# Kernel optimization log

Hardware: AMD Instinct MI355X
Metric: run time of the kernel (lower is better)

The kernel has to match this reference:

```python
import jax, jax.numpy as jnp
import numpy as np

N_NODES = 50000
N_EDGES = 800000
IN_DIM, HID_DIM, N_CLASS = 128, 128, 2
DROPOUT_P = 0.5
NEG_SLOPE = 0.01  # F.leaky_relu default


def gcn_conv(x, src, dst, W, b, n_nodes):
    """PyG GCNConv: add self-loops, sym-normalize, aggregate, then bias."""
    loops = jnp.arange(n_nodes, dtype=src.dtype)
    s = jnp.concatenate([src, loops])
    d = jnp.concatenate([dst, loops])
    # degree on A + I (edge weights = 1), counted at destination
    deg = jax.ops.segment_sum(jnp.ones_like(d, dtype=x.dtype), d, num_segments=n_nodes)
    dis = jnp.where(deg > 0, jax.lax.rsqrt(deg), 0.0)  # deg^{-1/2}
    norm = dis[s] * dis[d]                               # [E+N]
    h = x @ W                                            # [N, out]
    msg = h[s] * norm[:, None]                           # gather + scale
    out = jax.ops.segment_sum(msg, d, num_segments=n_nodes)  # scatter-add
    return out + b


def dropout(x, p, key):
    keep = 1.0 - p
    mask = jax.random.bernoulli(key, keep, x.shape)
    return jnp.where(mask, x / keep, 0.0)


def setup_inputs() -> dict:
    key = jax.random.key(0)
    ks = jax.random.split(key, 8)
    x = jax.random.normal(ks[0], (N_NODES, IN_DIM), dtype=jnp.float32)
    edge_index = jax.random.randint(ks[1], (2, N_EDGES), 0, N_NODES, dtype=jnp.int64)
    def glorot(k, fin, fout):
        lim = np.sqrt(6.0 / (fin + fout)).astype(np.float32)
        return jax.random.uniform(k, (fin, fout), jnp.float32, -lim, lim)
    W1 = glorot(ks[2], IN_DIM, HID_DIM)
    W2 = glorot(ks[3], HID_DIM, HID_DIM)
    W3 = glorot(ks[4], HID_DIM, N_CLASS)
    b1 = jnp.zeros((HID_DIM,), jnp.float32)
    b2 = jnp.zeros((HID_DIM,), jnp.float32)
    b3 = jnp.zeros((N_CLASS,), jnp.float32)
    return {"x": x, "edge_index": edge_index, "W1": W1, "b1": b1,
            "W2": W2, "b2": b2, "W3": W3, "b3": b3}


def reference(x, edge_index, W1, b1, W2, b2, W3, b3):
    src, dst = edge_index[0], edge_index[1]
    n = x.shape[0]
    dkey = jax.random.key(42)
    k1, k2 = jax.random.split(dkey)
    h = gcn_conv(x, src, dst, W1, b1, n)
    h = jax.nn.leaky_relu(h, NEG_SLOPE)
    h = dropout(h, DROPOUT_P, k1)
    h = gcn_conv(h, src, dst, W2, b2, n)
    h = jax.nn.leaky_relu(h, NEG_SLOPE)
    h = dropout(h, DROPOUT_P, k2)
    h = gcn_conv(h, src, dst, W3, b3, n)
    return jax.nn.log_softmax(h, axis=1)
```

## Files before the change

kernel.cpp:

```cpp
#include <hip/hip_runtime.h>
#include <stdint.h>

#define N_NODES 50000
#define N_EDGES 800000
#define DIM     128
#define NB   196
#define CAP  8192
#define CHUNK 2048
#define NBLK 391
#define GCAP 4096
#define G3NODES 128
#define G3CAP 4096
#define ZBLK 98

typedef __attribute__((ext_vector_type(8))) unsigned short ushort8_t;
typedef __attribute__((ext_vector_type(8))) short bfrag;
typedef __attribute__((ext_vector_type(4))) float f32x4;

__host__ __device__ inline void threefry2x32(uint32_t k0, uint32_t k1,
                                             uint32_t x0, uint32_t x1,
                                             uint32_t& o0, uint32_t& o1) {
    uint32_t ks0 = k0, ks1 = k1, ks2 = k0 ^ k1 ^ 0x1BD11BDAu;
    uint32_t v0 = x0 + ks0, v1 = x1 + ks1;
#define TF_R(r) { v0 += v1; v1 = (v1 << (r)) | (v1 >> (32 - (r))); v1 ^= v0; }
    TF_R(13) TF_R(15) TF_R(26) TF_R(6)
    v0 += ks1; v1 += ks2 + 1u;
    TF_R(17) TF_R(29) TF_R(16) TF_R(24)
    v0 += ks2; v1 += ks0 + 2u;
    TF_R(13) TF_R(15) TF_R(26) TF_R(6)
    v0 += ks0; v1 += ks1 + 3u;
    TF_R(17) TF_R(29) TF_R(16) TF_R(24)
    v0 += ks1; v1 += ks2 + 4u;
    TF_R(13) TF_R(15) TF_R(26) TF_R(6)
    v0 += ks2; v1 += ks0 + 5u;
#undef TF_R
    o0 = v0; o1 = v1;
}

__device__ inline float drop_scale(uint32_t kk0, uint32_t kk1, uint32_t i) {
    uint32_t b0, b1;
    threefry2x32(kk0, kk1, 0u, i, b0, b1);
    uint32_t bits = b0 ^ b1;
    return (bits >> 31) ? 0.0f : 2.0f;
}

__device__ inline float bf2f(ushort u) {
    return __uint_as_float(((uint32_t)u) << 16);
}

__device__ inline ushort f2bf_rne(float f) {
    uint32_t bits = __float_as_uint(f);
    uint32_t lsb = (bits >> 16) & 1u;
    bits += 0x7fffu + lsb;
    return (ushort)(bits >> 16);
}

template<int F32A, int SCALE>
__device__ inline void gemm_body(const ushort* __restrict__ Xb,
                                 const float* __restrict__ Xf,
                                 const ushort* __restrict__ Wt,
                                 const float* __restrict__ dis,
                                 ushort* __restrict__ Hb, int gb, int tid) {
    int w = tid >> 6, lane = tid & 63;
    int m0 = gb * 128 + w * 32;
    int lrow = lane & 15, quad = lane >> 4;
    f32x4 acc[2][8] = {};
    for (int kt = 0; kt < DIM; kt += 32) {
        bfrag a[2], b[8];
        #pragma unroll
        for (int t = 0; t < 2; ++t) {
            int m = m0 + t * 16 + lrow;
            if (m >= N_NODES) m = 0;
            if (F32A) {
                const float* p = Xf + (size_t)m * DIM + kt + quad * 8;
                f32x4 v0 = *(const f32x4*)p;
                f32x4 v1 = *(const f32x4*)(p + 4);
                #pragma unroll
                for (int j = 0; j < 4; ++j) {
                    a[t][j]     = (short)f2bf_rne(v0[j]);
                    a[t][j + 4] = (short)f2bf_rne(v1[j]);
                }
            } else {
                a[t] = *(const bfrag*)(Xb + (size_t)m * DIM + kt + quad * 8);
            }
        }
        #pragma unroll
        for (int c = 0; c < 8; ++c) {
            int n = c * 16 + lrow;
            b[c] = *(const bfrag*)(Wt + (size_t)n * DIM + kt + quad * 8);
        }
        #pragma unroll
        for (int t = 0; t < 2; ++t)
            #pragma unroll
            for (int c = 0; c < 8; ++c)
                acc[t][c] = __builtin_amdgcn_mfma_f32_16x16x32_bf16(a[t], b[c], acc[t][c], 0, 0, 0);
    }
    #pragma unroll
    for (int t = 0; t < 2; ++t) {
        #pragma unroll
        for (int r = 0; r < 4; ++r) {
            int rowi = m0 + t * 16 + quad * 4 + r;
            if (rowi < N_NODES) {
                float dv = SCALE ? dis[rowi] : 1.0f;
                #pragma unroll
                for (int c = 0; c < 8; ++c) {
                    int feat = c * 16 + lrow;
                    int fp = feat >> 5, off = feat & 31;
                    float z = SCALE ? acc[t][c][r] * dv : acc[t][c][r];
                    Hb[((size_t)fp * N_NODES + rowi) * 32 + off] = f2bf_rne(z);
                }
            }
        }
    }
}

__global__ __launch_bounds__(256) void k_prep(const float* __restrict__ W1,
                                              const float* __restrict__ W2,
                                              ushort* __restrict__ W1t,
                                              ushort* __restrict__ W2t,
                                              const int* __restrict__ src,
                                              const int* __restrict__ dst,
                                              uint32_t* __restrict__ gcur,
                                              uint32_t* __restrict__ packed,
                                              float* __restrict__ h3s) {
    __shared__ uint32_t h[NB];
    int b = blockIdx.x;
    int t = threadIdx.x;
    if (b < NBLK) {
        uint32_t dc[CHUNK / 256], sc[CHUNK / 256];
        if (t < NB) h[t] = 0u;
        __syncthreads();
        int base = b * CHUNK;
        #pragma unroll
        for (int i = 0; i < CHUNK / 256; ++i) {
            int e = base + i * 256 + t;
            if (e < N_EDGES) {
                dc[i] = (uint32_t)dst[e];
                sc[i] = (uint32_t)src[e];
                atomicAdd(&h[dc[i] >> 8], 1u);
            } else {
                dc[i] = 0xffffffffu;
            }
        }
        __syncthreads();
        if (t < NB) {
            uint32_t c = h[t];
            h[t] = c ? atomicAdd(&gcur[t], c) : 0u;
        }
        __syncthreads();
        #pragma unroll
        for (int i = 0; i < CHUNK / 256; ++i) {
            if (dc[i] != 0xffffffffu) {
                uint32_t d = dc[i];
                uint32_t s = sc[i];
                uint32_t bk = d >> 8;
                uint32_t pos = atomicAdd(&h[bk], 1u);
                if (pos < CAP)
                    packed[(size_t)bk * CAP + pos] = ((d & 255u) << 16) | s;
            }
        }
    } else if (b < NBLK + 128) {
        int j = (b - NBLK) * 256 + t;
        const float* W = (j < DIM * DIM) ? W1 : W2;
        ushort* Wt = (j < DIM * DIM) ? W1t : W2t;
        int i = j & (DIM * DIM - 1);
        int k = i >> 7, n = i & 127;
        Wt[n * DIM + k] = f2bf_rne(W[k * DIM + n]);
    } else {
        int idx = (b - NBLK - 128) * 256 + t;
        if (idx < (N_NODES * 2) / 4) {
            f32x4 z = {0.f, 0.f, 0.f, 0.f};
            ((f32x4*)h3s)[idx] = z;
        }
    }
}

__global__ __launch_bounds__(256) void k_fill(const uint32_t* __restrict__ gcur,
                                              const uint32_t* __restrict__ packed,
                                              uint32_t* __restrict__ row,
                                              float* __restrict__ dis,
                                              ushort* __restrict__ col16,
                                              const float* __restrict__ x,
                                              const ushort* __restrict__ W1t,
                                              ushort* __restrict__ Hb) {
    __shared__ uint32_t sdeg[256];
    __shared__ uint32_t scan[256];
    __shared__ uint32_t cur[256];
    int b = blockIdx.x;
    int t = threadIdx.x;
    if (b >= NB) {
        gemm_body<1, 0>(nullptr, x, W1t, nullptr, Hb, b - NB, t);
        return;
    }
    uint32_t n = gcur[b];
    scan[t] = (t < b) ? gcur[t] : 0u;
    __syncthreads();
    for (int off = 1; off < 256; off <<= 1) {
        uint32_t xx = (t >= off) ? scan[t - off] : 0u;
        __syncthreads();
        scan[t] += xx;
        __syncthreads();
    }
    uint32_t cbase = scan[255];
    __syncthreads();
    uint32_t pbase = (uint32_t)b * CAP;
    sdeg[t] = 0u;
    __syncthreads();
    for (uint32_t i = t; i < n; i += 256) {
        uint32_t u = packed[pbase + i];
        atomicAdd(&sdeg[u >> 16], 1u);
    }
    __syncthreads();
    uint32_t myd = sdeg[t];
    scan[t] = myd;
    __syncthreads();
    for (int off = 1; off < 256; off <<= 1) {
        uint32_t xx = (t >= off) ? scan[t - off] : 0u;
        __syncthreads();
        scan[t] += xx;
        __syncthreads();
    }
    uint32_t excl = scan[t] - myd;
    cur[t] = excl;
    int v = b * 256 + t;
    if (v <= N_NODES) row[v] = cbase + excl;
    if (v < N_NODES)  dis[v] = 1.0f / sqrtf((float)(myd + 1u));
    __syncthreads();
    for (uint32_t i = t; i < n; i += 256) {
        uint32_t u = packed[pbase + i];
        uint32_t pos = cbase + atomicAdd(&cur[u >> 16], 1u);
        col16[pos] = (ushort)(u & 0xffffu);
    }
}

template<int CLS, int SRCDIS>
__global__ __launch_bounds__(256) void k_gather_t(const uint32_t* __restrict__ row,
                                                  const ushort* __restrict__ col16,
                                                  const float* __restrict__ dis,
                                                  const ushort* __restrict__ Hb,
                                                  const float* __restrict__ bias,
                                                  ushort* __restrict__ OUTb,
                                                  const float* __restrict__ W3,
                                                  float* __restrict__ h3s,
                                                  uint32_t kk0, uint32_t kk1) {
    __shared__ ushort scol[GCAP];
    __shared__ uint32_t srow[65];
    int fp = blockIdx.x & 3;
    int c = blockIdx.x >> 2;
    int tid = threadIdx.x;
    int nbase = c * 64;
    int nend = nbase + 64; if (nend > N_NODES) nend = N_NODES;
    int nloc = nend - nbase;
    for (int i = tid; i <= nloc; i += 256) srow[i] = row[nbase + i];
    __syncthreads();
    uint32_t eLo = srow[0];
    uint32_t count = srow[nloc] - eLo;
    bool staged = count <= GCAP;
    if (staged) {
        for (uint32_t i = tid; i < count; i += 256) scol[i] = col16[eLo + i];
    }
    __syncthreads();

    int nl = tid >> 2;
    int q  = tid & 3;
    int v = nbase + nl;
    if (v >= N_NODES) return;
    float dv = dis[v];
    const ushort* Hf = Hb + (size_t)fp * N_NODES * 32;
    ushort8_t hv = *((const ushort8_t*)(Hf + (size_t)v * 32 + q * 8));
    float acc[8];
    #pragma unroll
    for (int j = 0; j < 8; ++j)
        acc[j] = SRCDIS ? dv * bf2f(hv[j]) : bf2f(hv[j]);

    uint32_t e0 = srow[nl] - eLo, e1 = srow[nl + 1] - eLo;
    uint32_t e = e0;
    if (staged) {
        for (; e + 4 <= e1; e += 4) {
            uint32_t s0 = scol[e], s1 = scol[e + 1], s2 = scol[e + 2], s3 = scol[e + 3];
            ushort8_t h0 = *((const ushort8_t*)(Hf + (size_t)s0 * 32 + q * 8));
            ushort8_t h1 = *((const ushort8_t*)(Hf + (size_t)s1 * 32 + q * 8));
            ushort8_t h2 = *((const ushort8_t*)(Hf + (size_t)s2 * 32 + q * 8));
            ushort8_t h3 = *((const ushort8_t*)(Hf + (size_t)s3 * 32 + q * 8));
            if (SRCDIS) {
                float d0 = dis[s0], d1 = dis[s1], d2 = dis[s2], d3 = dis[s3];
                #pragma unroll
                for (int j = 0; j < 8; ++j)
                    acc[j] += d0 * bf2f(h0[j]) + d1 * bf2f(h1[j])
                            + d2 * bf2f(h2[j]) + d3 * bf2f(h3[j]);
            } else {
                #pragma unroll
                for (int j = 0; j < 8; ++j)
                    acc[j] += (bf2f(h0[j]) + bf2f(h1[j])) + (bf2f(h2[j]) + bf2f(h3[j]));
            }
        }
        for (; e < e1; ++e) {
            uint32_t s0 = scol[e];
            ushort8_t h0 = *((const ushort8_t*)(Hf + (size_t)s0 * 32 + q * 8));
            float d0 = SRCDIS ? dis[s0] : 1.0f;
            #pragma unroll
            for (int j = 0; j < 8; ++j)
                acc[j] += SRCDIS ? d0 * bf2f(h0[j]) : bf2f(h0[j]);
        }
    } else {
        for (; e < e1; ++e) {
            uint32_t s0 = col16[eLo + e];
            ushort8_t h0 = *((const ushort8_t*)(Hf + (size_t)s0 * 32 + q * 8));
            float d0 = SRCDIS ? dis[s0] : 1.0f;
            #pragma unroll
            for (int j = 0; j < 8; ++j)
                acc[j] += SRCDIS ? d0 * bf2f(h0[j]) : bf2f(h0[j]);
        }
    }

    int cbase = fp * 32 + q * 8;
    uint32_t ibase = (uint32_t)(v * DIM + cbase);
    if (CLS == 0) {
        ushort8_t o;
        #pragma unroll
        for (int j = 0; j < 8; ++j) {
            float z = acc[j] * dv + bias[cbase + j];
            z = (z >= 0.f) ? z : 0.01f * z;
            z *= drop_scale(kk0, kk1, ibase + j);
            o[j] = f2bf_rne(z);
        }
        *((ushort8_t*)(OUTb + (size_t)v * DIM + cbase)) = o;
    } else {
        float o0 = 0.f, o1 = 0.f;
        #pragma unroll
        for (int j = 0; j < 8; ++j) {
            float z = acc[j] * dv + bias[cbase + j];
            z = (z >= 0.f) ? z : 0.01f * z;
            z *= drop_scale(kk0, kk1, ibase + j);
            o0 += z * W3[(cbase + j) * 2 + 0];
            o1 += z * W3[(cbase + j) * 2 + 1];
        }
        o0 += __shfl_xor(o0, 1); o0 += __shfl_xor(o0, 2);
        o1 += __shfl_xor(o1, 1); o1 += __shfl_xor(o1, 2);
        if (q == 0) {
            atomicAdd(&h3s[v * 2 + 0], o0 * dv);
            atomicAdd(&h3s[v * 2 + 1], o1 * dv);
        }
    }
}

__global__ __launch_bounds__(256) void k_gemm_bf16(const ushort* __restrict__ Xb,
                                                   const ushort* __restrict__ Wt,
                                                   const float* __restrict__ dis,
                                                   ushort* __restrict__ Hb) {
    gemm_body<0, 1>(Xb, nullptr, Wt, dis, Hb, blockIdx.x, threadIdx.x);
}

__global__ __launch_bounds__(256) void k_gather3(const uint32_t* __restrict__ row,
                                                 const ushort* __restrict__ col16,
                                                 const float* __restrict__ dis,
                                                 const float* __restrict__ H3s,
                                                 const float* __restrict__ b3,
                                                 float* __restrict__ out) {
    __shared__ ushort scol[G3CAP];
    __shared__ uint32_t srow[G3NODES + 1];
    int tid = threadIdx.x;
    int nbase = blockIdx.x * G3NODES;
    int nend = nbase + G3NODES; if (nend > N_NODES) nend = N_NODES;
    int nloc = nend - nbase;
    for (int i = tid; i <= nloc; i += 256) srow[i] = row[nbase + i];
    __syncthreads();
    uint32_t eLo = srow[0];
    uint32_t count = srow[nloc] - eLo;
    bool staged = count <= G3CAP;
    if (staged) {
        for (uint32_t i = tid; i < count; i += 256) scol[i] = col16[eLo + i];
    }
    __syncthreads();

    int nl = tid >> 1;
    int par = tid & 1;
    int v = nbase + nl;
    if (v >= N_NODES) return;
    const float2* H2 = (const float2*)H3s;
    float z0 = 0.f, z1 = 0.f;
    if (par == 0) {
        float2 h = H2[v];
        z0 = h.x; z1 = h.y;
    }
    uint32_t e0 = srow[nl] - eLo, e1 = srow[nl + 1] - eLo;
    if (staged) {
        for (uint32_t e = e0 + par; e < e1; e += 2) {
            float2 ha = H2[scol[e]];
            z0 += ha.x; z1 += ha.y;
        }
    } else {
        for (uint32_t e = e0 + par; e < e1; e += 2) {
            float2 ha = H2[col16[eLo + e]];
            z0 += ha.x; z1 += ha.y;
        }
    }
    z0 += __shfl_xor(z0, 1);
    z1 += __shfl_xor(z1, 1);
    if (par) return;
    float dv = dis[v];
    z0 = z0 * dv + b3[0];
    z1 = z1 * dv + b3[1];
    float m = fmaxf(z0, z1);
    float lse = m + logf(expf(z0 - m) + expf(z1 - m));
    out[v * 2 + 0] = z0 - lse;
    out[v * 2 + 1] = z1 - lse;
}

extern "C" void kernel_launch(void* const* d_in, const int* in_sizes, int n_in,
                              void* d_out, int out_size, void* d_ws, size_t ws_size,
                              hipStream_t stream) {
    const float* x  = (const float*)d_in[0];
    const int*   ei = (const int*)d_in[1];
    const float* W1 = (const float*)d_in[2];
    const float* b1 = (const float*)d_in[3];
    const float* W2 = (const float*)d_in[4];
    const float* b2 = (const float*)d_in[5];
    const float* W3 = (const float*)d_in[6];
    const float* b3 = (const float*)d_in[7];
    float* out = (float*)d_out;

    const int* src = ei;
    const int* dst = ei + N_EDGES;

    uint32_t* wsu = (uint32_t*)d_ws;
    float*    wsf = (float*)d_ws;
    uint32_t* gcur   = wsu;
    uint32_t* row    = wsu + 256;
    float*    dis    = wsf + 50304;
    uint32_t* packed = wsu + 100352;
    ushort*   col16  = (ushort*)(wsu + 1705984);
    ushort*   Hb     = (ushort*)(wsu + 2106112);
    ushort*   Bb     = (ushort*)(wsu + 8506112);
    ushort*   W1t    = (ushort*)(wsu + 11706112);
    ushort*   W2t    = (ushort*)(wsu + 11714304);
    float*    h3s    = wsf + 11722496;

    uint32_t k1a, k1b, k2a, k2b;
    threefry2x32(0u, 42u, 0u, 0u, k1a, k1b);
    threefry2x32(0u, 42u, 0u, 1u, k2a, k2b);

    hipMemsetAsync(gcur, 0, 256 * sizeof(uint32_t), stream);

    k_prep<<<NBLK + 128 + ZBLK, 256, 0, stream>>>(W1, W2, W1t, W2t,
                                                  src, dst, gcur, packed, h3s);

    k_fill<<<NB + 391, 256, 0, stream>>>(gcur, packed, row, dis, col16,
                                         x, W1t, Hb);

    int ggrid = ((N_NODES + 63) / 64) * 4;

    k_gather_t<0, 1><<<ggrid, 256, 0, stream>>>(row, col16, dis, Hb, b1, Bb,
                                                nullptr, nullptr, k1a, k1b);

    k_gemm_bf16<<<(N_NODES + 127) / 128, 256, 0, stream>>>(Bb, W2t, dis, Hb);
    k_gather_t<1, 0><<<ggrid, 256, 0, stream>>>(row, col16, dis, Hb, b2, nullptr,
                                                W3, h3s, k2a, k2b);

    k_gather3<<<(N_NODES + G3NODES - 1) / G3NODES, 256, 0, stream>>>(row, col16, dis,
                                                                     h3s, b3, out);
}
```

Baseline: 219.9 us.

## Split feature layout into 16-wide slices and split edges across thread pairs

The bf16 feature buffer changes from 4 slices of 32 features to 8 slices of 16 features, and the GEMM epilogue now writes in that layout. The gather grid doubles to 8 slices per 64-node chunk. Within a node, the 4 threads now cover 2 eight-feature quads times 2 edge parities, with partial sums combined by a lane shuffle. The aim is a smaller per-slice working set for better cache hit rates and more parallel edge loads per node. The cost is loading the CSR column indices twice as often and extra shuffle work in the epilogue.

```diff
diff --git a/kernel.cpp b/kernel.cpp
--- a/kernel.cpp
+++ b/kernel.cpp
@@ -12,6 +12,8 @@
 #define G3NODES 128
 #define G3CAP 4096
 #define ZBLK 98
+#define SLICES 8
+#define GCHUNKS 782
 
 typedef __attribute__((ext_vector_type(8))) unsigned short ushort8_t;
 typedef __attribute__((ext_vector_type(8))) short bfrag;
@@ -47,12 +49,27 @@
 __device__ inline float bf2f(ushort u) {
     return __uint_as_float(((uint32_t)u) << 16);
 }
+__device__ inline float bfpair_lo(uint32_t u) { return __uint_as_float(u << 16); }
+__device__ inline float bfpair_hi(uint32_t u) { return __uint_as_float(u & 0xffff0000u); }
 
 __device__ inline ushort f2bf_rne(float f) {
     uint32_t bits = __float_as_uint(f);
     uint32_t lsb = (bits >> 16) & 1u;
     bits += 0x7fffu + lsb;
     return (ushort)(bits >> 16);
+}
+
+__device__ inline void acc8(float* acc, uint4 u, float d) {
+    acc[0] += d * bfpair_lo(u.x); acc[1] += d * bfpair_hi(u.x);
+    acc[2] += d * bfpair_lo(u.y); acc[3] += d * bfpair_hi(u.y);
+    acc[4] += d * bfpair_lo(u.z); acc[5] += d * bfpair_hi(u.z);
+    acc[6] += d * bfpair_lo(u.w); acc[7] += d * bfpair_hi(u.w);
+}
+__device__ inline void acc8p(float* acc, uint4 u) {
+    acc[0] += bfpair_lo(u.x); acc[1] += bfpair_hi(u.x);
+    acc[2] += bfpair_lo(u.y); acc[3] += bfpair_hi(u.y);
+    acc[4] += bfpair_lo(u.z); acc[5] += bfpair_hi(u.z);
+    acc[6] += bfpair_lo(u.w); acc[7] += bfpair_hi(u.w);
 }
 
 template<int F32A, int SCALE>
@@ -104,10 +121,8 @@
                 float dv = SCALE ? dis[rowi] : 1.0f;
                 #pragma unroll
                 for (int c = 0; c < 8; ++c) {
-                    int feat = c * 16 + lrow;
-                    int fp = feat >> 5, off = feat & 31;
                     float z = SCALE ? acc[t][c][r] * dv : acc[t][c][r];
-                    Hb[((size_t)fp * N_NODES + rowi) * 32 + off] = f2bf_rne(z);
+                    Hb[((size_t)c * N_NODES + rowi) * 16 + lrow] = f2bf_rne(z);
                 }
             }
         }
@@ -245,8 +260,8 @@
                                                   uint32_t kk0, uint32_t kk1) {
     __shared__ ushort scol[GCAP];
     __shared__ uint32_t srow[65];
-    int fp = blockIdx.x & 3;
-    int c = blockIdx.x >> 2;
+    int sl = blockIdx.x & 7;
+    int c  = blockIdx.x >> 3;
     int tid = threadIdx.x;
     int nbase = c * 64;
     int nend = nbase + 64; if (nend > N_NODES) nend = N_NODES;
@@ -261,83 +276,85 @@
     }
     __syncthreads();
 
-    int nl = tid >> 2;
-    int q  = tid & 3;
+    int nl  = tid >> 2;
+    int q   = (tid >> 1) & 1;
+    int par = tid & 1;
     int v = nbase + nl;
     if (v >= N_NODES) return;
     float dv = dis[v];
-    const ushort* Hf = Hb + (size_t)fp * N_NODES * 32;
-    ushort8_t hv = *((const ushort8_t*)(Hf + (size_t)v * 32 + q * 8));
+    const ushort* Hf = Hb + (size_t)sl * N_NODES * 16;
     float acc[8];
     #pragma unroll
-    for (int j = 0; j < 8; ++j)
-        acc[j] = SRCDIS ? dv * bf2f(hv[j]) : bf2f(hv[j]);
-
-    uint32_t e0 = srow[nl] - eLo, e1 = srow[nl + 1] - eLo;
-    uint32_t e = e0;
+    for (int j = 0; j < 8; ++j) acc[j] = 0.f;
+    if (par == 0) {
+        uint4 u = *(const uint4*)(Hf + (size_t)v * 16 + q * 8);
+        acc8(acc, u, SRCDIS ? dv : 1.0f);
+    }
+
+    uint32_t e1 = srow[nl + 1] - eLo;
+    uint32_t e = (srow[nl] - eLo) + (uint32_t)par;
     if (staged) {
-        for (; e + 4 <= e1; e += 4) {
-            uint32_t s0 = scol[e], s1 = scol[e + 1], s2 = scol[e + 2], s3 = scol[e + 3];
-            ushort8_t h0 = *((const ushort8_t*)(Hf + (size_t)s0 * 32 + q * 8));
-            ushort8_t h1 = *((const ushort8_t*)(Hf + (size_t)s1 * 32 + q * 8));
-            ushort8_t h2 = *((const ushort8_t*)(Hf + (size_t)s2 * 32 + q * 8));
-            ushort8_t h3 = *((const ushort8_t*)(Hf + (size_t)s3 * 32 + q * 8));
+        for (; e + 6 < e1; e += 8) {
+            uint32_t s0 = scol[e], s1 = scol[e + 2], s2 = scol[e + 4], s3 = scol[e + 6];
+            uint4 u0 = *(const uint4*)(Hf + (size_t)s0 * 16 + q * 8);
+            uint4 u1 = *(const uint4*)(Hf + (size_t)s1 * 16 + q * 8);
+            uint4 u2 = *(const uint4*)(Hf + (size_t)s2 * 16 + q * 8);
+            uint4 u3 = *(const uint4*)(Hf + (size_t)s3 * 16 + q * 8);
             if (SRCDIS) {
                 float d0 = dis[s0], d1 = dis[s1], d2 = dis[s2], d3 = dis[s3];
-                #pragma unroll
-                for (int j = 0; j < 8; ++j)
-                    acc[j] += d0 * bf2f(h0[j]) + d1 * bf2f(h1[j])
-                            + d2 * bf2f(h2[j]) + d3 * bf2f(h3[j]);
+                acc8(acc, u0, d0); acc8(acc, u1, d1);
+                acc8(acc, u2, d2); acc8(acc, u3, d3);
             } else {
-                #pragma unroll
-                for (int j = 0; j < 8; ++j)
-                    acc[j] += (bf2f(h0[j]) + bf2f(h1[j])) + (bf2f(h2[j]) + bf2f(h3[j]));
+                acc8p(acc, u0); acc8p(acc, u1); acc8p(acc, u2); acc8p(acc, u3);
             }
         }
-        for (; e < e1; ++e) {
+        for (; e < e1; e += 2) {
             uint32_t s0 = scol[e];
-            ushort8_t h0 = *((const ushort8_t*)(Hf + (size_t)s0 * 32 + q * 8));
-            float d0 = SRCDIS ? dis[s0] : 1.0f;
-            #pragma unroll
-            for (int j = 0; j < 8; ++j)
-                acc[j] += SRCDIS ? d0 * bf2f(h0[j]) : bf2f(h0[j]);
+            uint4 u0 = *(const uint4*)(Hf + (size_t)s0 * 16 + q * 8);
+            if (SRCDIS) acc8(acc, u0, dis[s0]);
+            else        acc8p(acc, u0);
         }
     } else {
-        for (; e < e1; ++e) {
+        for (; e < e1; e += 2) {
             uint32_t s0 = col16[eLo + e];
-            ushort8_t h0 = *((const ushort8_t*)(Hf + (size_t)s0 * 32 + q * 8));
-            float d0 = SRCDIS ? dis[s0] : 1.0f;
-            #pragma unroll
-            for (int j = 0; j < 8; ++j)
-                acc[j] += SRCDIS ? d0 * bf2f(h0[j]) : bf2f(h0[j]);
-        }
-    }
-
-    int cbase = fp * 32 + q * 8;
-    uint32_t ibase = (uint32_t)(v * DIM + cbase);
+            uint4 u0 = *(const uint4*)(Hf + (size_t)s0 * 16 + q * 8);
+            if (SRCDIS) acc8(acc, u0, dis[s0]);
+            else        acc8p(acc, u0);
+        }
+    }
+
+    #pragma unroll
+    for (int j = 0; j < 8; ++j) acc[j] += __shfl_xor(acc[j], 1);
+
+    int jb = par * 4;
+    int cb = sl * 16 + q * 8 + jb;
+    uint32_t ib = (uint32_t)(v * DIM + cb);
     if (CLS == 0) {
-        ushort8_t o;
-        #pragma unroll
-        for (int j = 0; j < 8; ++j) {
-            float z = acc[j] * dv + bias[cbase + j];
-            z = (z >= 0.f) ? z : 0.01f * z;
-            z *= drop_scale(kk0, kk1, ibase + j);
-            o[j] = f2bf_rne(z);
-        }
-        *((ushort8_t*)(OUTb + (size_t)v * DIM + cbase)) = o;
+        ushort4 o;
+        float z0 = acc[jb + 0] * dv + bias[cb + 0];
+        float z1 = acc[jb + 1] * dv + bias[cb + 1];
+        float z2 = acc[jb + 2] * dv + bias[cb + 2];
+        float z3 = acc[jb + 3] * dv + bias[cb + 3];
+        z0 = (z0 >= 0.f) ? z0 : 0.01f * z0;  z0 *= drop_scale(kk0, kk1, ib + 0);
+        z1 = (z1 >= 0.f) ? z1 : 0.01f * z1;  z1 *= drop_scale(kk0, kk1, ib + 1);
+        z2 = (z2 >= 0.f) ? z2 : 0.01f * z2;  z2 *= drop_scale(kk0, kk1, ib + 2);
+        z3 = (z3 >= 0.f) ? z3 : 0.01f * z3;  z3 *= drop_scale(kk0, kk1, ib + 3);
+        o.x = f2bf_rne(z0); o.y = f2bf_rne(z1);
+        o.z = f2bf_rne(z2); o.w = f2bf_rne(z3);
+        *((ushort4*)(OUTb + (size_t)v * DIM + cb)) = o;
     } else {
         float o0 = 0.f, o1 = 0.f;
         #pragma unroll
-        for (int j = 0; j < 8; ++j) {
-            float z = acc[j] * dv + bias[cbase + j];
+        for (int jj = 0; jj < 4; ++jj) {
+            float z = acc[jb + jj] * dv + bias[cb + jj];
             z = (z >= 0.f) ? z : 0.01f * z;
-            z *= drop_scale(kk0, kk1, ibase + j);
-            o0 += z * W3[(cbase + j) * 2 + 0];
-            o1 += z * W3[(cbase + j) * 2 + 1];
+            z *= drop_scale(kk0, kk1, ib + jj);
+            o0 += z * W3[(cb + jj) * 2 + 0];
+            o1 += z * W3[(cb + jj) * 2 + 1];
         }
         o0 += __shfl_xor(o0, 1); o0 += __shfl_xor(o0, 2);
         o1 += __shfl_xor(o1, 1); o1 += __shfl_xor(o1, 2);
-        if (q == 0) {
+        if ((tid & 3) == 0) {
             atomicAdd(&h3s[v * 2 + 0], o0 * dv);
             atomicAdd(&h3s[v * 2 + 1], o1 * dv);
         }
@@ -448,7 +465,7 @@
     k_fill<<<NB + 391, 256, 0, stream>>>(gcur, packed, row, dis, col16,
                                          x, W1t, Hb);
 
-    int ggrid = ((N_NODES + 63) / 64) * 4;
+    int ggrid = GCHUNKS * SLICES;
 
     k_gather_t<0, 1><<<ggrid, 256, 0, stream>>>(row, col16, dis, Hb, b1, Bb,
                                                 nullptr, nullptr, k1a, k1b);
```

After: 243.5 us. 1.11x slower.

## Switch hidden features to row-major layout and gather full rows per node

Applied to the files above, without the earlier changes.

The GEMM epilogue now writes the hidden features in plain row-major [node][128] order instead of four 32-feature planes. The gather kernel is reorganised to match: each block handles 16 nodes, with 16 threads per node covering all 128 features. Each neighbour row is now fetched as one contiguous 256-byte read, the edge list is staged in shared memory once instead of once per plane, and the neighbour loop is unrolled by eight. In exchange there are many more, smaller blocks, and the class-3 projection needs a wider shuffle reduction across the 16 threads of a node.

```diff
diff --git a/kernel.cpp b/kernel.cpp
--- a/kernel.cpp
+++ b/kernel.cpp
@@ -8,7 +8,9 @@
 #define CAP  8192
 #define CHUNK 2048
 #define NBLK 391
-#define GCAP 4096
+#define GNODES 16
+#define GGRID 3125
+#define GCAP 2048
 #define G3NODES 128
 #define G3CAP 4096
 #define ZBLK 98
@@ -47,12 +49,27 @@
 __device__ inline float bf2f(ushort u) {
     return __uint_as_float(((uint32_t)u) << 16);
 }
+__device__ inline float bfpair_lo(uint32_t u) { return __uint_as_float(u << 16); }
+__device__ inline float bfpair_hi(uint32_t u) { return __uint_as_float(u & 0xffff0000u); }
 
 __device__ inline ushort f2bf_rne(float f) {
     uint32_t bits = __float_as_uint(f);
     uint32_t lsb = (bits >> 16) & 1u;
     bits += 0x7fffu + lsb;
     return (ushort)(bits >> 16);
+}
+
+__device__ inline void acc8(float* acc, uint4 u, float d) {
+    acc[0] += d * bfpair_lo(u.x); acc[1] += d * bfpair_hi(u.x);
+    acc[2] += d * bfpair_lo(u.y); acc[3] += d * bfpair_hi(u.y);
+    acc[4] += d * bfpair_lo(u.z); acc[5] += d * bfpair_hi(u.z);
+    acc[6] += d * bfpair_lo(u.w); acc[7] += d * bfpair_hi(u.w);
+}
+__device__ inline void acc8p(float* acc, uint4 u) {
+    acc[0] += bfpair_lo(u.x); acc[1] += bfpair_hi(u.x);
+    acc[2] += bfpair_lo(u.y); acc[3] += bfpair_hi(u.y);
+    acc[4] += bfpair_lo(u.z); acc[5] += bfpair_hi(u.z);
+    acc[6] += bfpair_lo(u.w); acc[7] += bfpair_hi(u.w);
 }
 
 template<int F32A, int SCALE>
@@ -105,9 +122,8 @@
                 #pragma unroll
                 for (int c = 0; c < 8; ++c) {
                     int feat = c * 16 + lrow;
-                    int fp = feat >> 5, off = feat & 31;
                     float z = SCALE ? acc[t][c][r] * dv : acc[t][c][r];
-                    Hb[((size_t)fp * N_NODES + rowi) * 32 + off] = f2bf_rne(z);
+                    Hb[(size_t)rowi * DIM + feat] = f2bf_rne(z);
                 }
             }
         }
@@ -244,76 +260,95 @@
                                                   float* __restrict__ h3s,
                                                   uint32_t kk0, uint32_t kk1) {
     __shared__ ushort scol[GCAP];
-    __shared__ uint32_t srow[65];
-    int fp = blockIdx.x & 3;
-    int c = blockIdx.x >> 2;
+    __shared__ uint32_t srow[GNODES + 1];
     int tid = threadIdx.x;
-    int nbase = c * 64;
-    int nend = nbase + 64; if (nend > N_NODES) nend = N_NODES;
-    int nloc = nend - nbase;
-    for (int i = tid; i <= nloc; i += 256) srow[i] = row[nbase + i];
+    int nbase = blockIdx.x * GNODES;
+    if (tid <= GNODES) srow[tid] = row[nbase + tid];
     __syncthreads();
     uint32_t eLo = srow[0];
-    uint32_t count = srow[nloc] - eLo;
+    uint32_t count = srow[GNODES] - eLo;
     bool staged = count <= GCAP;
     if (staged) {
         for (uint32_t i = tid; i < count; i += 256) scol[i] = col16[eLo + i];
     }
     __syncthreads();
 
-    int nl = tid >> 2;
-    int q  = tid & 3;
+    int nl = tid >> 4;
+    int q  = tid & 15;
     int v = nbase + nl;
-    if (v >= N_NODES) return;
     float dv = dis[v];
-    const ushort* Hf = Hb + (size_t)fp * N_NODES * 32;
-    ushort8_t hv = *((const ushort8_t*)(Hf + (size_t)v * 32 + q * 8));
     float acc[8];
-    #pragma unroll
-    for (int j = 0; j < 8; ++j)
-        acc[j] = SRCDIS ? dv * bf2f(hv[j]) : bf2f(hv[j]);
+    {
+        uint4 u = *(const uint4*)(Hb + (size_t)v * DIM + q * 8);
+        acc[0] = bfpair_lo(u.x); acc[1] = bfpair_hi(u.x);
+        acc[2] = bfpair_lo(u.y); acc[3] = bfpair_hi(u.y);
+        acc[4] = bfpair_lo(u.z); acc[5] = bfpair_hi(u.z);
+        acc[6] = bfpair_lo(u.w); acc[7] = bfpair_hi(u.w);
+        if (SRCDIS) {
+            #pragma unroll
+            for (int j = 0; j < 8; ++j) acc[j] *= dv;
+        }
+    }
 
     uint32_t e0 = srow[nl] - eLo, e1 = srow[nl + 1] - eLo;
     uint32_t e = e0;
     if (staged) {
-        for (; e + 4 <= e1; e += 4) {
-            uint32_t s0 = scol[e], s1 = scol[e + 1], s2 = scol[e + 2], s3 = scol[e + 3];
-            ushort8_t h0 = *((const ushort8_t*)(Hf + (size_t)s0 * 32 + q * 8));
-            ushort8_t h1 = *((const ushort8_t*)(Hf + (size_t)s1 * 32 + q * 8));
-            ushort8_t h2 = *((const ushort8_t*)(Hf + (size_t)s2 * 32 + q * 8));
-            ushort8_t h3 = *((const ushort8_t*)(Hf + (size_t)s3 * 32 + q * 8));
+        for (; e + 8 <= e1; e += 8) {
+            uint32_t s0 = scol[e],     s1 = scol[e + 1];
+            uint32_t s2 = scol[e + 2], s3 = scol[e + 3];
+            uint32_t s4 = scol[e + 4], s5 = scol[e + 5];
+            uint32_t s6 = scol[e + 6], s7 = scol[e + 7];
+            uint4 u0 = *(const uint4*)(Hb + (size_t)s0 * DIM + q * 8);
+            uint4 u1 = *(const uint4*)(Hb + (size_t)s1 * DIM + q * 8);
+            uint4 u2 = *(const uint4*)(Hb + (size_t)s2 * DIM + q * 8);
+            uint4 u3 = *(const uint4*)(Hb + (size_t)s3 * DIM + q * 8);
+            uint4 u4 = *(const uint4*)(Hb + (size_t)s4 * DIM + q * 8);
+            uint4 u5 = *(const uint4*)(Hb + (size_t)s5 * DIM + q * 8);
+            uint4 u6 = *(const uint4*)(Hb + (size_t)s6 * DIM + q * 8);
+            uint4 u7 = *(const uint4*)(Hb + (size_t)s7 * DIM + q * 8);
             if (SRCDIS) {
                 float d0 = dis[s0], d1 = dis[s1], d2 = dis[s2], d3 = dis[s3];
-                #pragma unroll
-                for (int j = 0; j < 8; ++j)
-                    acc[j] += d0 * bf2f(h0[j]) + d1 * bf2f(h1[j])
-                            + d2 * bf2f(h2[j]) + d3 * bf2f(h3[j]);
+                float d4 = dis[s4], d5 = dis[s5], d6 = dis[s6], d7 = dis[s7];
+                acc8(acc, u0, d0); acc8(acc, u1, d1);
+                acc8(acc, u2, d2); acc8(acc, u3, d3);
+                acc8(acc, u4, d4); acc8(acc, u5, d5);
+                acc8(acc, u6, d6); acc8(acc, u7, d7);
             } else {
-                #pragma unroll
-                for (int j = 0; j < 8; ++j)
-                    acc[j] += (bf2f(h0[j]) + bf2f(h1[j])) + (bf2f(h2[j]) + bf2f(h3[j]));
+                acc8p(acc, u0); acc8p(acc, u1); acc8p(acc, u2); acc8p(acc, u3);
+                acc8p(acc, u4); acc8p(acc, u5); acc8p(acc, u6); acc8p(acc, u7);
+            }
+        }
+        for (; e + 4 <= e1; e += 4) {
+            uint32_t s0 = scol[e],     s1 = scol[e + 1];
+            uint32_t s2 = scol[e + 2], s3 = scol[e + 3];
+            uint4 u0 = *(const uint4*)(Hb + (size_t)s0 * DIM + q * 8);
+            uint4 u1 = *(const uint4*)(Hb + (size_t)s1 * DIM + q * 8);
+            uint4 u2 = *(const uint4*)(Hb + (size_t)s2 * DIM + q * 8);
+            uint4 u3 = *(const uint4*)(Hb + (size_t)s3 * DIM + q * 8);
+            if (SRCDIS) {
+                float d0 = dis[s0], d1 = dis[s1], d2 = dis[s2], d3 = dis[s3];
+                acc8(acc, u0, d0); acc8(acc, u1, d1);
+                acc8(acc, u2, d2); acc8(acc, u3, d3);
+            } else {
+                acc8p(acc, u0); acc8p(acc, u1); acc8p(acc, u2); acc8p(acc, u3);
             }
         }
         for (; e < e1; ++e) {
             uint32_t s0 = scol[e];
-            ushort8_t h0 = *((const ushort8_t*)(Hf + (size_t)s0 * 32 + q * 8));
-            float d0 = SRCDIS ? dis[s0] : 1.0f;
-            #pragma unroll
-            for (int j = 0; j < 8; ++j)
-                acc[j] += SRCDIS ? d0 * bf2f(h0[j]) : bf2f(h0[j]);
+            uint4 u0 = *(const uint4*)(Hb + (size_t)s0 * DIM + q * 8);
+            if (SRCDIS) acc8(acc, u0, dis[s0]);
+            else        acc8p(acc, u0);
         }
     } else {
         for (; e < e1; ++e) {
             uint32_t s0 = col16[eLo + e];
-            ushort8_t h0 = *((const ushort8_t*)(Hf + (size_t)s0 * 32 + q * 8));
-            float d0 = SRCDIS ? dis[s0] : 1.0f;
-            #pragma unroll
-            for (int j = 0; j < 8; ++j)
-                acc[j] += SRCDIS ? d0 * bf2f(h0[j]) : bf2f(h0[j]);
-        }
-    }
-
-    int cbase = fp * 32 + q * 8;
+            uint4 u0 = *(const uint4*)(Hb + (size_t)s0 * DIM + q * 8);
+            if (SRCDIS) acc8(acc, u0, dis[s0]);
+            else        acc8p(acc, u0);
+        }
+    }
+
+    int cbase = q * 8;
     uint32_t ibase = (uint32_t)(v * DIM + cbase);
     if (CLS == 0) {
         ushort8_t o;
@@ -336,7 +371,9 @@
             o1 += z * W3[(cbase + j) * 2 + 1];
         }
         o0 += __shfl_xor(o0, 1); o0 += __shfl_xor(o0, 2);
+        o0 += __shfl_xor(o0, 4); o0 += __shfl_xor(o0, 8);
         o1 += __shfl_xor(o1, 1); o1 += __shfl_xor(o1, 2);
+        o1 += __shfl_xor(o1, 4); o1 += __shfl_xor(o1, 8);
         if (q == 0) {
             atomicAdd(&h3s[v * 2 + 0], o0 * dv);
             atomicAdd(&h3s[v * 2 + 1], o1 * dv);
@@ -448,13 +485,11 @@
     k_fill<<<NB + 391, 256, 0, stream>>>(gcur, packed, row, dis, col16,
                                          x, W1t, Hb);
 
-    int ggrid = ((N_NODES + 63) / 64) * 4;
-
-    k_gather_t<0, 1><<<ggrid, 256, 0, stream>>>(row, col16, dis, Hb, b1, Bb,
+    k_gather_t<0, 1><<<GGRID, 256, 0, stream>>>(row, col16, dis, Hb, b1, Bb,
                                                 nullptr, nullptr, k1a, k1b);
 
     k_gemm_bf16<<<(N_NODES + 127) / 128, 256, 0, stream>>>(Bb, W2t, dis, Hb);
-    k_gather_t<1, 0><<<ggrid, 256, 0, stream>>>(row, col16, dis, Hb, b2, nullptr,
+    k_gather_t<1, 0><<<GGRID, 256, 0, stream>>>(row, col16, dis, Hb, b2, nullptr,
                                                 W3, h3s, k2a, k2b);
 
     k_gather3<<<(N_NODES + G3NODES - 1) / G3NODES, 256, 0, stream>>>(row, col16, dis,
```

Result: faster. 213.9 us (-2.8%).
